# Optimization experiments

Hardware: AMD Instinct MI355X
Metric: run time of the kernel (lower is better)

The kernel has to match this reference:

```python
import jax, jax.numpy as jnp
import numpy as np


def setup_inputs() -> dict:
    key = jax.random.key(0)
    k1, k2, k3, k4 = jax.random.split(key, 4)
    return {
        "src_feat1": jax.random.normal(k1, (4, 1024, 64, 64), dtype=jnp.float32),
        "tar_feat1": jax.random.normal(k2, (4, 1024, 64, 64), dtype=jnp.float32),
        "src_feat2": jax.random.normal(k3, (4, 2048, 32, 32), dtype=jnp.float32),
        "tar_feat2": jax.random.normal(k4, (4, 2048, 32, 32), dtype=jnp.float32),
    }


def _nn_concat(src, tar):
    # src: [B,C,H1,W1], tar: [B,C,H2,W2] -> [B,2C,H1,W1]
    B, C, H, W = src.shape
    s = src.reshape(B, C, -1).transpose(0, 2, 1)   # [B,N1,C]
    t = tar.reshape(B, C, -1).transpose(0, 2, 1)   # [B,N2,C]
    # squared euclidean distance (argmin of d^2 == argmin of d, sqrt monotonic)
    d2 = (
        jnp.sum(s * s, axis=-1, keepdims=True)      # [B,N1,1]
        + jnp.sum(t * t, axis=-1)[:, None, :]       # [B,1,N2]
        - 2.0 * jnp.einsum("bnc,bmc->bnm", s, t)    # [B,N1,N2]
    )
    idx = jnp.argmin(d2, axis=2)                    # [B,N1]
    nearest = jnp.take_along_axis(t, idx[..., None], axis=1)  # [B,N1,C]
    nearest = nearest.transpose(0, 2, 1).reshape(B, C, H, W)
    return jnp.concatenate([src, nearest], axis=1)


def reference(src_feat1, tar_feat1, src_feat2, tar_feat2):
    c1 = _nn_concat(src_feat1, tar_feat1)           # [B,2048,64,64]
    c2 = _nn_concat(src_feat2, tar_feat2)           # [B,4096,32,32]
    B, C2 = c2.shape[:2]
    H1, W1 = c1.shape[2], c1.shape[3]
    # F.interpolate(mode='bilinear', align_corners=False) == jax.image.resize 'linear'
    c2r = jax.image.resize(c2, (B, C2, H1, W1), method="linear")
    return jnp.concatenate([c1, c2r], axis=1)       # [B,6144,64,64]
```

## Files before the change

### kernel.cpp

```cpp
#include <hip/hip_runtime.h>
#include <cstdint>

using u8 = unsigned char;
using u64 = unsigned long long;

typedef _Float16 f16x8 __attribute__((ext_vector_type(8)));
typedef float f32x4 __attribute__((ext_vector_type(4)));
typedef unsigned short u16x8 __attribute__((ext_vector_type(8)));

__device__ __forceinline__ void gload16(const void* g, void* l) {
  __builtin_amdgcn_global_load_lds((const __attribute__((address_space(1))) void*)g,
                                   (__attribute__((address_space(3))) void*)l, 16, 0, 0);
}

#define VMCNT(N) asm volatile("s_waitcnt vmcnt(" #N ")" ::: "memory")

__device__ __forceinline__ void split_body(const float* __restrict__ in,
                                           _Float16* __restrict__ hi,
                                           _Float16* __restrict__ lo,
                                           float* __restrict__ hnp,
                                           int C, int N, int NC,
                                           int cblk, int nblk, int b, bool with_hn) {
  const int n = nblk * 256 + (int)threadIdx.x;
  const int c0 = cblk * 32;
  const float* inB = in + (size_t)b * C * N;
  f16x8 hv[4], lv[4];
  float ss = 0.f;
#pragma unroll
  for (int g = 0; g < 4; ++g)
#pragma unroll
    for (int e = 0; e < 8; ++e) {
      float x = inB[(size_t)(c0 + g * 8 + e) * N + n];
      _Float16 h = (_Float16)x;
      float r = (x - (float)h) * 4096.f;
      hv[g][e] = h;
      lv[g][e] = (_Float16)r;
      ss = fmaf(x, x, ss);
    }
  _Float16* oh = hi + ((size_t)b * N + n) * C + c0;
  _Float16* ol = lo + ((size_t)b * N + n) * C + c0;
#pragma unroll
  for (int g = 0; g < 4; ++g) {
    *(f16x8*)(oh + g * 8) = hv[g];
    *(f16x8*)(ol + g * 8) = lv[g];
  }
  if (with_hn) hnp[((size_t)b * NC + cblk) * N + n] = ss;
}

__global__ __launch_bounds__(256) void prep_all(
    const float* __restrict__ s1, const float* __restrict__ t1,
    const float* __restrict__ s2, const float* __restrict__ t2,
    _Float16* __restrict__ h1s, _Float16* __restrict__ l1s,
    _Float16* __restrict__ h1t, _Float16* __restrict__ l1t,
    _Float16* __restrict__ h2s, _Float16* __restrict__ l2s,
    _Float16* __restrict__ h2t, _Float16* __restrict__ l2t,
    float* __restrict__ hnp1, float* __restrict__ hnp2) {
  const int f = (int)blockIdx.x;
  if (f < 4096) {
    const bool isT = f >= 2048;
    const int local = f & 2047;
    const int cblk = local & 31;
    const int r = local >> 5;
    const int nblk = r & 15, b = r >> 4;
    split_body(isT ? t1 : s1, isT ? h1t : h1s, isT ? l1t : l1s, hnp1,
               1024, 4096, 32, cblk, nblk, b, isT);
  } else {
    const int l0 = f - 4096;
    const bool isT = l0 >= 1024;
    const int local = l0 & 1023;
    const int cblk = local & 63;
    const int r = local >> 6;
    const int nblk = r & 3, b = r >> 2;
    split_body(isT ? t2 : s2, isT ? h2t : h2s, isT ? l2t : l2s, hnp2,
               2048, 1024, 64, cblk, nblk, b, isT);
  }
}

__global__ __launch_bounds__(256) void hn_all(const float* __restrict__ hnp1,
                                              const float* __restrict__ hnp2,
                                              float* __restrict__ hn1,
                                              float* __restrict__ hn2) {
  const int x = (int)blockIdx.x, b = (int)blockIdx.y;
  if (x < 16) {
    const int n = x * 256 + (int)threadIdx.x;
    float a = 0.f;
    for (int cc = 0; cc < 32; ++cc) a += hnp1[((size_t)b * 32 + cc) * 4096 + n];
    hn1[(size_t)b * 4096 + n] = 0.5f * a;
  } else {
    const int n = (x - 16) * 256 + (int)threadIdx.x;
    float a = 0.f;
    for (int cc = 0; cc < 64; ++cc) a += hnp2[((size_t)b * 64 + cc) * 1024 + n];
    hn2[(size_t)b * 1024 + n] = 0.5f * a;
  }
}

#define MFMA_BLOCK(GI)                                                         \
  __builtin_amdgcn_s_barrier();                                                \
  asm volatile("s_waitcnt lgkmcnt(0)" ::: "memory");                           \
  __builtin_amdgcn_sched_barrier(0);                                           \
  __builtin_amdgcn_s_setprio(1);                                               \
  _Pragma("unroll") for (int i2 = 0; i2 < 4; ++i2)                             \
      _Pragma("unroll") for (int j = 0; j < NJ; ++j) acc[(GI)*4 + i2][j] =     \
      __builtin_amdgcn_mfma_f32_16x16x32_f16(av[i2], bv[j],                    \
                                             acc[(GI)*4 + i2][j], 0, 0, 0);    \
  __builtin_amdgcn_s_setprio(0);                                               \
  asm volatile("" ::: "memory");                                               \
  __builtin_amdgcn_s_barrier();

__device__ __forceinline__ void filter_body(
    const u8* __restrict__ Ahi, const u8* __restrict__ Bhi,
    const float* __restrict__ hn, unsigned short* __restrict__ sc,
    int M, int N, int NT, int mbase, int nbase, int b, u8* smem) {
  constexpr int MI = 8, NJ = 4;
  constexpr int BM = 256;
  constexpr int CHUNK_A = BM * 64;
  constexpr int CHUNK = 2 * CHUNK_A;
  constexpr int NTH = 512;

  const int tid = threadIdx.x;
  const int lane = tid & 63;
  const int wid = tid >> 6;
  const int wrow = wid >> 2;
  const int wcol = wid & 3;
  const int lr = lane & 15, kh = lane >> 4;
  const size_t rstride = (size_t)NT * 128;

  const int r0 = (tid >> 6) * 16 + ((tid & 63) >> 2);
  const int sA = ((lane & 3) ^ (r0 >> 1)) & 3;
  const u8* aP0 = Ahi + ((size_t)b * M + mbase + r0) * rstride + sA * 16;
  const u8* aP1 = aP0 + (size_t)(NTH / 4) * rstride;
  const u8* bP0 = Bhi + ((size_t)b * N + nbase + r0) * rstride + sA * 16;
  const u8* bP1 = bP0 + (size_t)(NTH / 4) * rstride;

  auto STAGE = [&](int X, int h) {
    const size_t ko = (size_t)X * 128 + h * 64;
    u8* cb = smem + ((X & 1) * 2 + h) * CHUNK;
    gload16(aP0 + ko, cb + tid * 16);
    gload16(aP1 + ko, cb + NTH * 16 + tid * 16);
    gload16(bP0 + ko, cb + CHUNK_A + tid * 16);
    gload16(bP1 + ko, cb + CHUNK_A + NTH * 16 + tid * 16);
  };

  int a_off[MI], b_off[NJ];
#pragma unroll
  for (int i = 0; i < MI; ++i) {
    const int row = wrow * (MI * 16) + i * 16 + lr;
    a_off[i] = row * 64 + (((kh ^ (row >> 1)) & 3) << 4);
  }
#pragma unroll
  for (int j = 0; j < NJ; ++j) {
    const int row = wcol * (NJ * 16) + j * 16 + lr;
    b_off[j] = CHUNK_A + row * 64 + (((kh ^ (row >> 1)) & 3) << 4);
  }

  f32x4 acc[MI][NJ];
#pragma unroll
  for (int i = 0; i < MI; ++i)
#pragma unroll
    for (int j = 0; j < NJ; ++j) acc[i][j] = f32x4{0.f, 0.f, 0.f, 0.f};

  STAGE(0, 0);
  STAGE(0, 1);
  STAGE(1, 0);
  VMCNT(8);
  __builtin_amdgcn_s_barrier();

  for (int X = 0; X < NT; ++X) {
    const u8* cb0 = smem + ((X & 1) * 2) * CHUNK;
    const u8* cb1 = cb0 + CHUNK;
    f16x8 av[4], bv[NJ];

#pragma unroll
    for (int j = 0; j < NJ; ++j) bv[j] = *(const f16x8*)(cb0 + b_off[j]);
#pragma unroll
    for (int i2 = 0; i2 < 4; ++i2) av[i2] = *(const f16x8*)(cb0 + a_off[i2]);
    if (X + 1 < NT) STAGE(X + 1, 1);
    if (X + 1 < NT) { VMCNT(8); } else { VMCNT(0); }
    MFMA_BLOCK(0)

#pragma unroll
    for (int i2 = 0; i2 < 4; ++i2) av[i2] = *(const f16x8*)(cb0 + a_off[4 + i2]);
    MFMA_BLOCK(1)

#pragma unroll
    for (int j = 0; j < NJ; ++j) bv[j] = *(const f16x8*)(cb1 + b_off[j]);
#pragma unroll
    for (int i2 = 0; i2 < 4; ++i2) av[i2] = *(const f16x8*)(cb1 + a_off[i2]);
    if (X + 2 < NT) STAGE(X + 2, 0);
    if (X + 1 < NT) {
      if (X + 2 < NT) { VMCNT(8); } else { VMCNT(4); }
    }
    MFMA_BLOCK(0)

#pragma unroll
    for (int i2 = 0; i2 < 4; ++i2) av[i2] = *(const f16x8*)(cb1 + a_off[4 + i2]);
    MFMA_BLOCK(1)
  }

  const float* hnB = hn + (size_t)b * N;
  float hnv[NJ];
  int ncol[NJ];
#pragma unroll
  for (int j = 0; j < NJ; ++j) {
    ncol[j] = nbase + wcol * (NJ * 16) + j * 16 + lr;
    hnv[j] = hnB[ncol[j]];
  }
  unsigned short* scB = sc + (size_t)b * M * N;
#pragma unroll
  for (int i = 0; i < MI; ++i)
#pragma unroll
    for (int r = 0; r < 4; ++r) {
      const int m = mbase + wrow * (MI * 16) + i * 16 + kh * 4 + r;
      unsigned short* srow = scB + (size_t)m * N;
#pragma unroll
      for (int j = 0; j < NJ; ++j) {
        float score = hnv[j] - acc[i][j][r];
        int qi = (int)(score * 64.0f);
        qi = qi < 0 ? 0 : (qi > 65535 ? 65535 : qi);
        srow[ncol[j]] = (unsigned short)qi;
      }
    }
}

__global__ __launch_bounds__(512, 2) void nn_filter_all(
    const u8* __restrict__ A1, const u8* __restrict__ B1,
    const float* __restrict__ hn1, unsigned short* __restrict__ sc1,
    const u8* __restrict__ A2, const u8* __restrict__ B2,
    const float* __restrict__ hn2, unsigned short* __restrict__ sc2) {
  __shared__ u8 smem[4 * 32768];
  const int bid = (int)blockIdx.x;
  if (bid < 64) {
    const int sbid = (bid & 7) * 8 + (bid >> 3);
    const int b = sbid >> 4;
    const int rr = sbid & 15;
    const int n1 = rr & 3;
    const int mb = rr >> 2;
    filter_body(A2, B2, hn2, sc2, 1024, 1024, 32, mb * 256, n1 * 256, b, smem);
  } else {
    const int l = bid - 64;
    const int sbid = (l & 7) * 128 + (l >> 3);
    const int perB = 256;
    const int b = sbid / perB;
    const int rr = sbid - b * perB;
    const int n1 = rr & 3;
    const int t2 = rr >> 2;
    const int mb = t2 & 15;
    const int n2 = t2 >> 4;
    filter_body(A1, B1, hn1, sc1, 4096, 4096, 16, mb * 256, (n2 * 4 + n1) * 256, b, smem);
  }
}

template <int K, int CH>
__device__ __forceinline__ void select_body(
    const unsigned short* __restrict__ sc,
    const _Float16* __restrict__ hiA, const _Float16* __restrict__ loA,
    const _Float16* __restrict__ hiB, const _Float16* __restrict__ loB,
    const float* __restrict__ hn, unsigned* __restrict__ idx,
    int M, int N, int rowblk, int b) {
  const int w = threadIdx.x >> 6, lane = threadIdx.x & 63;
  const int row = rowblk * 4 + w;
  const unsigned short* q = sc + ((size_t)b * M + row) * N;

  unsigned cm[CH];
#pragma unroll
  for (int ch = 0; ch < CH; ++ch) {
    u16x8 v = *(const u16x8*)(q + ch * 512 + lane * 8);
    unsigned m0 = v[0] < v[1] ? v[0] : v[1];
    unsigned m1 = v[2] < v[3] ? v[2] : v[3];
    unsigned m2 = v[4] < v[5] ? v[4] : v[5];
    unsigned m3 = v[6] < v[7] ? v[6] : v[7];
    m0 = m0 < m1 ? m0 : m1;
    m2 = m2 < m3 ? m2 : m3;
    unsigned m = m0 < m2 ? m0 : m2;
#pragma unroll
    for (int off = 32; off >= 1; off >>= 1) {
      unsigned o = (unsigned)__shfl_xor((int)m, off);
      m = o < m ? o : m;
    }
    cm[ch] = m;
  }
  unsigned mn = 0xFFFFu;
#pragma unroll
  for (int ch = 0; ch < CH; ++ch) mn = cm[ch] < mn ? cm[ch] : mn;
  const unsigned thr = mn + 64;

  constexpr int PER = K / 64;
  const float inv = 2.44140625e-4f;
  float sv[PER];
  const _Float16* hA = hiA + ((size_t)b * M + row) * K;
  const _Float16* lA = loA + ((size_t)b * M + row) * K;
#pragma unroll
  for (int i = 0; i < PER; ++i)
    sv[i] = fmaf((float)lA[i * 64 + lane], inv, (float)hA[i * 64 + lane]);

  float bestv = 3.4e38f;
  int bestn = 0x7FFFFFFF;
  const float* hnB = hn + (size_t)b * N;
#pragma unroll
  for (int ch = 0; ch < CH; ++ch) {
    if (cm[ch] > thr) continue;
    u16x8 v = *(const u16x8*)(q + ch * 512 + lane * 8);
#pragma unroll
    for (int e = 0; e < 8; ++e) {
      u64 mask = __ballot((unsigned)v[e] <= thr);
      while (mask) {
        int bit = __ffsll((long long)mask) - 1;
        mask &= mask - 1;
        int n = ch * 512 + bit * 8 + e;
        const _Float16* hB = hiB + ((size_t)b * N + n) * K;
        const _Float16* lB = loB + ((size_t)b * N + n) * K;
        float part = 0.f;
#pragma unroll
        for (int i = 0; i < PER; ++i)
          part = fmaf(sv[i], fmaf((float)lB[i * 64 + lane], inv, (float)hB[i * 64 + lane]), part);
#pragma unroll
        for (int off = 32; off >= 1; off >>= 1) part += __shfl_xor(part, off);
        float scf = hnB[n] - part;
        if (scf < bestv || (scf == bestv && n < bestn)) { bestv = scf; bestn = n; }
      }
    }
  }
  if (lane == 0) idx[(size_t)b * M + row] = (unsigned)bestn;
}

__global__ __launch_bounds__(256) void select_all(
    const unsigned short* __restrict__ sc1,
    const _Float16* __restrict__ h1s, const _Float16* __restrict__ l1s,
    const _Float16* __restrict__ h1t, const _Float16* __restrict__ l1t,
    const float* __restrict__ hn1, unsigned* __restrict__ idx1,
    const unsigned short* __restrict__ sc2,
    const _Float16* __restrict__ h2s, const _Float16* __restrict__ l2s,
    const _Float16* __restrict__ h2t, const _Float16* __restrict__ l2t,
    const float* __restrict__ hn2, unsigned* __restrict__ idx2) {
  const int x = (int)blockIdx.x, b = (int)blockIdx.y;
  if (x < 1024)
    select_body<1024, 8>(sc1, h1s, l1s, h1t, l1t, hn1, idx1, 4096, 4096, x, b);
  else
    select_body<2048, 2>(sc2, h2s, l2s, h2t, l2t, hn2, idx2, 1024, 1024, x - 1024, b);
}

__global__ __launch_bounds__(256) void finalize(
    const float* __restrict__ src1, const float* __restrict__ tar1,
    const float* __restrict__ src2, const float* __restrict__ tar2,
    const unsigned* __restrict__ idx1, const unsigned* __restrict__ idx2,
    float* __restrict__ out) {
  const int b = blockIdx.y;
  int c = (int)blockIdx.x;
  if (c < 2048) {
    float* orow = out + ((size_t)b * 6144 + c) * 4096;
    if (c < 1024) {
      const float4* s4 = (const float4*)(src1 + ((size_t)b * 1024 + c) * 4096);
      float4* o4 = (float4*)orow;
#pragma unroll
      for (int i = 0; i < 4; ++i) o4[threadIdx.x + i * 256] = s4[threadIdx.x + i * 256];
    } else {
      const float* trow = tar1 + ((size_t)b * 1024 + (c - 1024)) * 4096;
      const unsigned* ib = idx1 + (size_t)b * 4096;
      for (int p = threadIdx.x; p < 4096; p += 256) orow[p] = trow[ib[p]];
    }
    return;
  }
  c -= 2048;
  __shared__ float row[1024];
  if (c < 2048) {
    const float* in = src2 + ((size_t)b * 2048 + c) * 1024;
    for (int p = threadIdx.x; p < 1024; p += 256) row[p] = in[p];
  } else {
    const float* trow = tar2 + ((size_t)b * 2048 + (c - 2048)) * 1024;
    const unsigned* ib = idx2 + (size_t)b * 1024;
    for (int p = threadIdx.x; p < 1024; p += 256) row[p] = trow[ib[p]];
  }
  __syncthreads();
  float* orow = out + ((size_t)b * 6144 + 2048 + c) * 4096;
  for (int q = threadIdx.x; q < 4096; q += 256) {
    int y = q >> 6, x = q & 63;
    int ky = y >> 1, kx = x >> 1;
    int y0, y1, x0, x1;
    float wy0, wy1, wx0, wx1;
    if (y & 1) { y0 = ky; y1 = (ky + 1 < 32) ? ky + 1 : 31; wy0 = 0.75f; wy1 = 0.25f; }
    else       { y0 = (ky > 0) ? ky - 1 : 0; y1 = ky;       wy0 = 0.25f; wy1 = 0.75f; }
    if (x & 1) { x0 = kx; x1 = (kx + 1 < 32) ? kx + 1 : 31; wx0 = 0.75f; wx1 = 0.25f; }
    else       { x0 = (kx > 0) ? kx - 1 : 0; x1 = kx;       wx0 = 0.25f; wx1 = 0.75f; }
    float v = wy0 * (wx0 * row[y0 * 32 + x0] + wx1 * row[y0 * 32 + x1]) +
              wy1 * (wx0 * row[y1 * 32 + x0] + wx1 * row[y1 * 32 + x1]);
    orow[q] = v;
  }
}

extern "C" void kernel_launch(void* const* d_in, const int* in_sizes, int n_in,
                              void* d_out, int out_size, void* d_ws, size_t ws_size,
                              hipStream_t stream) {
  const float* src1 = (const float*)d_in[0];
  const float* tar1 = (const float*)d_in[1];
  const float* src2 = (const float*)d_in[2];
  const float* tar2 = (const float*)d_in[3];
  float* out = (float*)d_out;

  u8* scratch = (u8*)d_out;
  _Float16* hi1s = (_Float16*)scratch;
  _Float16* lo1s = (_Float16*)(scratch + (32ull << 20));
  _Float16* hi1t = (_Float16*)(scratch + (64ull << 20));
  _Float16* lo1t = (_Float16*)(scratch + (96ull << 20));
  _Float16* hi2s = (_Float16*)(scratch + (128ull << 20));
  _Float16* lo2s = (_Float16*)(scratch + (144ull << 20));
  _Float16* hi2t = (_Float16*)(scratch + (160ull << 20));
  _Float16* lo2t = (_Float16*)(scratch + (176ull << 20));
  unsigned short* sc1 = (unsigned short*)(scratch + (192ull << 20));
  unsigned short* sc2 = (unsigned short*)(scratch + (320ull << 20));
  float* hnp1 = (float*)(scratch + (328ull << 20));
  float* hnp2 = (float*)(scratch + (331ull << 20));

  float* hn1 = (float*)d_ws;
  float* hn2 = hn1 + 4 * 4096;
  unsigned* idx1 = (unsigned*)(hn2 + 4 * 1024);
  unsigned* idx2 = idx1 + 4 * 4096;

  prep_all<<<6144, 256, 0, stream>>>(src1, tar1, src2, tar2,
                                     hi1s, lo1s, hi1t, lo1t,
                                     hi2s, lo2s, hi2t, lo2t, hnp1, hnp2);
  hn_all<<<dim3(20, 4), 256, 0, stream>>>(hnp1, hnp2, hn1, hn2);

  nn_filter_all<<<1088, 512, 0, stream>>>(
      (const u8*)hi1s, (const u8*)hi1t, hn1, sc1,
      (const u8*)hi2s, (const u8*)hi2t, hn2, sc2);

  select_all<<<dim3(1280, 4), 256, 0, stream>>>(
      sc1, hi1s, lo1s, hi1t, lo1t, hn1, idx1,
      sc2, hi2s, lo2s, hi2t, lo2t, hn2, idx2);

  finalize<<<dim3(6144, 4), 256, 0, stream>>>(src1, tar1, src2, tar2, idx1, idx2, out);
}
```

Before: 536.1 us.

## Store 8-bit tile-relative filter scores with per-tile row minima

The filter kernel now reduces each row's quantized score minimum per 256-column tile, writes that minimum to a small side array, and stores scores as saturated 8-bit deltas from it instead of 16-bit values. The select kernel reads the tile minima to form the threshold directly, skipping the first full pass over the score row, and scans 16 bytes per lane using per-tile limits. The intent is to halve score-matrix write and read traffic and remove one scan in select. In exchange it adds a shared-memory reduction and extra barriers in the filter epilogue. Saturating deltas at 255 is safe because the threshold window of 64 stays below the clamp.

```diff
diff --git a/kernel.cpp b/kernel.cpp
--- a/kernel.cpp
+++ b/kernel.cpp
@@ -6,7 +6,7 @@
 
 typedef _Float16 f16x8 __attribute__((ext_vector_type(8)));
 typedef float f32x4 __attribute__((ext_vector_type(4)));
-typedef unsigned short u16x8 __attribute__((ext_vector_type(8)));
+typedef unsigned char u8x16 __attribute__((ext_vector_type(16)));
 
 __device__ __forceinline__ void gload16(const void* g, void* l) {
   __builtin_amdgcn_global_load_lds((const __attribute__((address_space(1))) void*)g,
@@ -107,9 +107,12 @@
   asm volatile("" ::: "memory");                                               \
   __builtin_amdgcn_s_barrier();
 
+constexpr unsigned DELTA_Q = 64;
+
 __device__ __forceinline__ void filter_body(
     const u8* __restrict__ Ahi, const u8* __restrict__ Bhi,
-    const float* __restrict__ hn, unsigned short* __restrict__ sc,
+    const float* __restrict__ hn, u8* __restrict__ sc,
+    unsigned short* __restrict__ g_tmin, int nTiles,
     int M, int N, int NT, int mbase, int nbase, int b, u8* smem) {
   constexpr int MI = 8, NJ = 4;
   constexpr int BM = 256;
@@ -198,6 +201,7 @@
   }
 
   const float* hnB = hn + (size_t)b * N;
+  const int tileIdx = nbase >> 8;
   float hnv[NJ];
   int ncol[NJ];
 #pragma unroll
@@ -205,28 +209,69 @@
     ncol[j] = nbase + wcol * (NJ * 16) + j * 16 + lr;
     hnv[j] = hnB[ncol[j]];
   }
-  unsigned short* scB = sc + (size_t)b * M * N;
+
+  auto quant = [&](int i, int j, int r) -> unsigned {
+    float s = hnv[j] - acc[i][j][r];
+    int qi = (int)(s * 64.0f);
+    return (unsigned)(qi < 0 ? 0 : (qi > 65535 ? 65535 : qi));
+  };
+
+  unsigned* lmin = (unsigned*)smem;
+  unsigned* tminL = lmin + 256 * 4;
+
 #pragma unroll
   for (int i = 0; i < MI; ++i)
 #pragma unroll
     for (int r = 0; r < 4; ++r) {
-      const int m = mbase + wrow * (MI * 16) + i * 16 + kh * 4 + r;
-      unsigned short* srow = scB + (size_t)m * N;
+      unsigned rq = 0xFFFFFFFFu;
 #pragma unroll
       for (int j = 0; j < NJ; ++j) {
-        float score = hnv[j] - acc[i][j][r];
-        int qi = (int)(score * 64.0f);
-        qi = qi < 0 ? 0 : (qi > 65535 ? 65535 : qi);
-        srow[ncol[j]] = (unsigned short)qi;
+        unsigned q = quant(i, j, r);
+        rq = q < rq ? q : rq;
+      }
+#pragma unroll
+      for (int off = 1; off <= 8; off <<= 1) {
+        unsigned o = (unsigned)__shfl_xor((int)rq, off);
+        rq = o < rq ? o : rq;
+      }
+      if (lr == 0) lmin[(wrow * 128 + i * 16 + kh * 4 + r) * 4 + wcol] = rq;
+    }
+  __syncthreads();
+  for (int m = tid; m < 256; m += NTH) {
+    unsigned t = lmin[m * 4];
+#pragma unroll
+    for (int w = 1; w < 4; ++w) {
+      unsigned o = lmin[m * 4 + w];
+      t = o < t ? o : t;
+    }
+    tminL[m] = t;
+    g_tmin[((size_t)b * M + mbase + m) * nTiles + tileIdx] = (unsigned short)t;
+  }
+  __syncthreads();
+  u8* scB = sc + (size_t)b * M * N;
+#pragma unroll
+  for (int i = 0; i < MI; ++i)
+#pragma unroll
+    for (int r = 0; r < 4; ++r) {
+      const int ml = wrow * 128 + i * 16 + kh * 4 + r;
+      const unsigned tm = tminL[ml];
+      u8* srow = scB + (size_t)(mbase + ml) * N;
+#pragma unroll
+      for (int j = 0; j < NJ; ++j) {
+        unsigned d = quant(i, j, r) - tm;
+        d = d > 255u ? 255u : d;
+        srow[ncol[j]] = (u8)d;
       }
     }
 }
 
 __global__ __launch_bounds__(512, 2) void nn_filter_all(
     const u8* __restrict__ A1, const u8* __restrict__ B1,
-    const float* __restrict__ hn1, unsigned short* __restrict__ sc1,
+    const float* __restrict__ hn1, u8* __restrict__ sc1,
+    unsigned short* __restrict__ tmin1,
     const u8* __restrict__ A2, const u8* __restrict__ B2,
-    const float* __restrict__ hn2, unsigned short* __restrict__ sc2) {
+    const float* __restrict__ hn2, u8* __restrict__ sc2,
+    unsigned short* __restrict__ tmin2) {
   __shared__ u8 smem[4 * 32768];
   const int bid = (int)blockIdx.x;
   if (bid < 64) {
@@ -235,7 +280,7 @@
     const int rr = sbid & 15;
     const int n1 = rr & 3;
     const int mb = rr >> 2;
-    filter_body(A2, B2, hn2, sc2, 1024, 1024, 32, mb * 256, n1 * 256, b, smem);
+    filter_body(A2, B2, hn2, sc2, tmin2, 4, 1024, 1024, 32, mb * 256, n1 * 256, b, smem);
   } else {
     const int l = bid - 64;
     const int sbid = (l & 7) * 128 + (l >> 3);
@@ -246,43 +291,30 @@
     const int t2 = rr >> 2;
     const int mb = t2 & 15;
     const int n2 = t2 >> 4;
-    filter_body(A1, B1, hn1, sc1, 4096, 4096, 16, mb * 256, (n2 * 4 + n1) * 256, b, smem);
-  }
-}
-
-template <int K, int CH>
+    filter_body(A1, B1, hn1, sc1, tmin1, 16, 4096, 4096, 16, mb * 256, (n2 * 4 + n1) * 256, b, smem);
+  }
+}
+
+template <int K, int NTILES>
 __device__ __forceinline__ void select_body(
-    const unsigned short* __restrict__ sc,
+    const u8* __restrict__ q8, const unsigned short* __restrict__ g_tmin,
     const _Float16* __restrict__ hiA, const _Float16* __restrict__ loA,
     const _Float16* __restrict__ hiB, const _Float16* __restrict__ loB,
     const float* __restrict__ hn, unsigned* __restrict__ idx,
     int M, int N, int rowblk, int b) {
   const int w = threadIdx.x >> 6, lane = threadIdx.x & 63;
   const int row = rowblk * 4 + w;
-  const unsigned short* q = sc + ((size_t)b * M + row) * N;
-
-  unsigned cm[CH];
-#pragma unroll
-  for (int ch = 0; ch < CH; ++ch) {
-    u16x8 v = *(const u16x8*)(q + ch * 512 + lane * 8);
-    unsigned m0 = v[0] < v[1] ? v[0] : v[1];
-    unsigned m1 = v[2] < v[3] ? v[2] : v[3];
-    unsigned m2 = v[4] < v[5] ? v[4] : v[5];
-    unsigned m3 = v[6] < v[7] ? v[6] : v[7];
-    m0 = m0 < m1 ? m0 : m1;
-    m2 = m2 < m3 ? m2 : m3;
-    unsigned m = m0 < m2 ? m0 : m2;
-#pragma unroll
-    for (int off = 32; off >= 1; off >>= 1) {
-      unsigned o = (unsigned)__shfl_xor((int)m, off);
-      m = o < m ? o : m;
-    }
-    cm[ch] = m;
-  }
-  unsigned mn = 0xFFFFu;
-#pragma unroll
-  for (int ch = 0; ch < CH; ++ch) mn = cm[ch] < mn ? cm[ch] : mn;
-  const unsigned thr = mn + 64;
+  const u8* q = q8 + ((size_t)b * M + row) * N;
+  const unsigned short* tmr = g_tmin + ((size_t)b * M + row) * NTILES;
+
+  unsigned tm = 0xFFFFu;
+  if (lane < NTILES) tm = tmr[lane];
+#pragma unroll
+  for (int off = 32; off >= 1; off >>= 1) {
+    unsigned o = (unsigned)__shfl_xor((int)tm, off);
+    tm = o < tm ? o : tm;
+  }
+  const int thr = (int)tm + (int)DELTA_Q;
 
   constexpr int PER = K / 64;
   const float inv = 2.44140625e-4f;
@@ -296,17 +328,26 @@
   float bestv = 3.4e38f;
   int bestn = 0x7FFFFFFF;
   const float* hnB = hn + (size_t)b * N;
-#pragma unroll
-  for (int ch = 0; ch < CH; ++ch) {
-    if (cm[ch] > thr) continue;
-    u16x8 v = *(const u16x8*)(q + ch * 512 + lane * 8);
-#pragma unroll
-    for (int e = 0; e < 8; ++e) {
-      u64 mask = __ballot((unsigned)v[e] <= thr);
-      while (mask) {
-        int bit = __ffsll((long long)mask) - 1;
-        mask &= mask - 1;
-        int n = ch * 512 + bit * 8 + e;
+  constexpr int CH = K == 0 ? 1 : 1;
+  const int nch = N >> 10;
+  for (int ch = 0; ch < nch; ++ch) {
+    const int n0 = ch * 1024 + lane * 16;
+    const int lim = thr - (int)tmr[n0 >> 8];
+    u8x16 v = *(const u8x16*)(q + n0);
+    unsigned hit = 0;
+#pragma unroll
+    for (int e = 0; e < 16; ++e)
+      if ((int)v[e] <= lim) hit |= 1u << e;
+    u64 lm = __ballot(hit != 0);
+    while (lm) {
+      int src = __ffsll((long long)lm) - 1;
+      lm &= lm - 1;
+      unsigned h = (unsigned)__shfl((int)hit, src);
+      const int nb = ch * 1024 + src * 16;
+      while (h) {
+        int e = __ffs((int)h) - 1;
+        h &= h - 1;
+        int n = nb + e;
         const _Float16* hB = hiB + ((size_t)b * N + n) * K;
         const _Float16* lB = loB + ((size_t)b * N + n) * K;
         float part = 0.f;
@@ -324,19 +365,19 @@
 }
 
 __global__ __launch_bounds__(256) void select_all(
-    const unsigned short* __restrict__ sc1,
+    const u8* __restrict__ sc1, const unsigned short* __restrict__ tmin1,
     const _Float16* __restrict__ h1s, const _Float16* __restrict__ l1s,
     const _Float16* __restrict__ h1t, const _Float16* __restrict__ l1t,
     const float* __restrict__ hn1, unsigned* __restrict__ idx1,
-    const unsigned short* __restrict__ sc2,
+    const u8* __restrict__ sc2, const unsigned short* __restrict__ tmin2,
     const _Float16* __restrict__ h2s, const _Float16* __restrict__ l2s,
     const _Float16* __restrict__ h2t, const _Float16* __restrict__ l2t,
     const float* __restrict__ hn2, unsigned* __restrict__ idx2) {
   const int x = (int)blockIdx.x, b = (int)blockIdx.y;
   if (x < 1024)
-    select_body<1024, 8>(sc1, h1s, l1s, h1t, l1t, hn1, idx1, 4096, 4096, x, b);
+    select_body<1024, 16>(sc1, tmin1, h1s, l1s, h1t, l1t, hn1, idx1, 4096, 4096, x, b);
   else
-    select_body<2048, 2>(sc2, h2s, l2s, h2t, l2t, hn2, idx2, 1024, 1024, x - 1024, b);
+    select_body<2048, 4>(sc2, tmin2, h2s, l2s, h2t, l2t, hn2, idx2, 1024, 1024, x - 1024, b);
 }
 
 __global__ __launch_bounds__(256) void finalize(
@@ -405,10 +446,12 @@
   _Float16* lo2s = (_Float16*)(scratch + (144ull << 20));
   _Float16* hi2t = (_Float16*)(scratch + (160ull << 20));
   _Float16* lo2t = (_Float16*)(scratch + (176ull << 20));
-  unsigned short* sc1 = (unsigned short*)(scratch + (192ull << 20));
-  unsigned short* sc2 = (unsigned short*)(scratch + (320ull << 20));
-  float* hnp1 = (float*)(scratch + (328ull << 20));
-  float* hnp2 = (float*)(scratch + (331ull << 20));
+  u8* sc1 = scratch + (192ull << 20);
+  u8* sc2 = scratch + (256ull << 20);
+  unsigned short* tmin1 = (unsigned short*)(scratch + (261ull << 20));
+  unsigned short* tmin2 = (unsigned short*)(scratch + (262ull << 20));
+  float* hnp1 = (float*)(scratch + (263ull << 20));
+  float* hnp2 = (float*)(scratch + (266ull << 20));
 
   float* hn1 = (float*)d_ws;
   float* hn2 = hn1 + 4 * 4096;
@@ -421,12 +464,12 @@
   hn_all<<<dim3(20, 4), 256, 0, stream>>>(hnp1, hnp2, hn1, hn2);
 
   nn_filter_all<<<1088, 512, 0, stream>>>(
-      (const u8*)hi1s, (const u8*)hi1t, hn1, sc1,
-      (const u8*)hi2s, (const u8*)hi2t, hn2, sc2);
+      (const u8*)hi1s, (const u8*)hi1t, hn1, sc1, tmin1,
+      (const u8*)hi2s, (const u8*)hi2t, hn2, sc2, tmin2);
 
   select_all<<<dim3(1280, 4), 256, 0, stream>>>(
-      sc1, hi1s, lo1s, hi1t, lo1t, hn1, idx1,
-      sc2, hi2s, lo2s, hi2t, lo2t, hn2, idx2);
+      sc1, tmin1, hi1s, lo1s, hi1t, lo1t, hn1, idx1,
+      sc2, tmin2, hi2s, lo2s, hi2t, lo2t, hn2, idx2);
 
   finalize<<<dim3(6144, 4), 256, 0, stream>>>(src1, tar1, src2, tar2, idx1, idx2, out);
 }
```

Result: slower. 593.4 us (+10.7%).
